# Optimization experiments

Measured on AMD Instinct MI355X. Metric: run time of the kernel, lower is better.

Reference implementation:

```python
import jax, jax.numpy as jnp
import numpy as np

ALPHA = 10.0   # args.alpha softmax sharpness
EPS = 1e-8     # torch CosineSimilarity eps


def setup_inputs() -> dict:
    key = jax.random.key(0)
    k0, k1, k2, k3 = jax.random.split(key, 4)
    B, S, F, D, C = 8, 1024, 32, 128, 16
    Hs = jax.random.normal(k0, (B, S, F, D), dtype=jnp.float32)
    Cj = jax.random.normal(k1, (C, D), dtype=jnp.float32)
    W = jax.random.normal(k2, (D, D), dtype=jnp.float32) * 0.05  # nn.Linear weight [out,in]
    b = jnp.zeros((D,), dtype=jnp.float32)
    importance = jax.random.uniform(k3, (B, S, F), dtype=jnp.float32)
    return {"Hs": Hs, "Cj": Cj, "W": W, "b": b, "importance": importance}


def reference(Hs, Cj, W, b, importance):
    # Hs: [B,S,F,D] features; Cj: [C,D] cluster centers; importance: [B,S,F]
    # Faithful to Model_DTSSOCC.assignment (importance is not None branch),
    # but avoids materializing the broadcasted [B,S,F,C,D] repeat tensors.
    Hn = Hs / jnp.maximum(jnp.linalg.norm(Hs, axis=-1, keepdims=True), EPS)
    Cn = Cj / jnp.maximum(jnp.linalg.norm(Cj, axis=-1, keepdims=True), EPS)
    cos = jnp.einsum('bsfd,cd->bsfc', Hn, Cn)            # cosine_sim4 over dim D
    logits = -ALPHA * 0.5 * (1.0 - cos)                  # -alpha * dists, [B,S,F,C]
    w3 = jax.nn.softmax(logits, axis=3)                  # softmax over centers
    w = jax.nn.softmax(logits, axis=2)                   # softmax over feas
    w3 = jnp.swapaxes(w3, 2, 3)                          # [B,S,C,F]
    w = jnp.swapaxes(w, 2, 3)                            # [B,S,C,F]
    F_tj = jax.nn.relu(jnp.einsum('bsfd,ed->bsfe', Hs, W) + b)  # relu(Linear(F_t))
    # importance update: bmm(w3, importance) then softmax over centers
    imp = jax.nn.softmax(jnp.einsum('bscf,bsf->bsc', w3, importance), axis=2)
    # weighted feature aggregation: bmm(w, F_tj) -> [B,S,C,D]
    f_t_new = jnp.einsum('bscf,bsfd->bscd', w, F_tj)
    return f_t_new, imp
```

## Files before the change

### kernel.cpp

```cpp
#include <hip/hip_runtime.h>
#include <hip/hip_bf16.h>
#include <math.h>

constexpr int Bn = 8, Sn = 1024, Fn = 32, Dn = 128, Cc = 16;
constexpr int NSITE = Bn * Sn;

#define EPSV 1e-8f

typedef __attribute__((ext_vector_type(8))) short bf16x8;
typedef __attribute__((ext_vector_type(4))) short bf16x4;
typedef __attribute__((ext_vector_type(4))) float f32x4;

__device__ inline short f2bf(float x) {
    __hip_bfloat16 h = __float2bfloat16(x);
    short s;
    __builtin_memcpy(&s, &h, sizeof(s));
    return s;
}

__device__ inline bf16x8 cvt8(f32x4 x0, f32x4 x1) {
    bf16x8 r;
    r[0] = f2bf(x0[0]); r[1] = f2bf(x0[1]); r[2] = f2bf(x0[2]); r[3] = f2bf(x0[3]);
    r[4] = f2bf(x1[0]); r[5] = f2bf(x1[1]); r[6] = f2bf(x1[2]); r[7] = f2bf(x1[3]);
    return r;
}

__global__ void prep_kernel(const float* __restrict__ Cj,
                            const float* __restrict__ W,
                            short* __restrict__ CnPack,
                            short* __restrict__ Wb) {
    const int tid = threadIdx.x;
    if (blockIdx.x < 64) {
        int t = blockIdx.x * 256 + tid;
        int n = t >> 7, k = t & 127;
        short v = f2bf(W[n * Dn + k]);
        int frag = (n >> 4) * 4 + (k >> 5);
        int lane = ((k >> 3) & 3) * 16 + (n & 15);
        Wb[(frag * 64 + lane) * 8 + (k & 7)] = v;
    } else {
        int c = blockIdx.x - 64;
        __shared__ float part[2];
        float v = 0.f, sq = 0.f;
        if (tid < 128) {
            v = Cj[c * Dn + tid];
            sq = v * v;
            #pragma unroll
            for (int off = 32; off > 0; off >>= 1) sq += __shfl_down(sq, off);
        }
        if (tid < 128 && (tid & 63) == 0) part[tid >> 6] = sq;
        __syncthreads();
        if (tid < 128) {
            float cn = v / fmaxf(sqrtf(part[0] + part[1]), EPSV);
            int kt = tid >> 5, ln = ((tid >> 3) & 3) * 16 + c, j = tid & 7;
            CnPack[(kt * 64 + ln) * 8 + j] = f2bf(cn);
        }
    }
}

__launch_bounds__(64, 4)
__global__ void site_kernel(const float* __restrict__ Hs,
                            const short* __restrict__ CnPack,
                            const short* __restrict__ Wb,
                            const float* __restrict__ bvec,
                            const float* __restrict__ imp_in,
                            float* __restrict__ f_out,
                            float* __restrict__ imp_out) {
    __shared__ __align__(16) short F_tjT[128][40];

    const int lane = threadIdx.x;
    const int c16  = lane & 15;
    const int g    = lane >> 4;
    const int site = blockIdx.x;

    const float* hsrc = Hs + (size_t)site * (Fn * Dn);
    const f32x4 zro = {0.f, 0.f, 0.f, 0.f};

    f32x4 x[16];
    #pragma unroll
    for (int kt = 0; kt < 4; ++kt) {
        const f32x4* p0 = (const f32x4*)(hsrc + c16 * Dn + kt * 32 + g * 8);
        const f32x4* p1 = (const f32x4*)(hsrc + (16 + c16) * Dn + kt * 32 + g * 8);
        x[4 * kt + 0] = p0[0];
        x[4 * kt + 1] = p0[1];
        x[4 * kt + 2] = p1[0];
        x[4 * kt + 3] = p1[1];
    }
    bf16x8 bcf[4];
    #pragma unroll
    for (int kt = 0; kt < 4; ++kt)
        bcf[kt] = *(const bf16x8*)&CnPack[(kt * 64 + lane) * 8];
    const float* impp = imp_in + (size_t)site * Fn;
    f32x4 impv0 = *(const f32x4*)(impp + 4 * g);
    f32x4 impv1 = *(const f32x4*)(impp + 16 + 4 * g);

    bf16x8 aF[2][4];
    #pragma unroll
    for (int kt = 0; kt < 4; ++kt) {
        aF[0][kt] = cvt8(x[4 * kt + 0], x[4 * kt + 1]);
        aF[1][kt] = cvt8(x[4 * kt + 2], x[4 * kt + 3]);
    }

    f32x4 gm0 = zro, gm1 = zro, cos0 = zro, cos1 = zro;
    #pragma unroll
    for (int kt = 0; kt < 4; ++kt) {
        gm0  = __builtin_amdgcn_mfma_f32_16x16x32_bf16(aF[0][kt], aF[0][kt], gm0, 0, 0, 0);
        gm1  = __builtin_amdgcn_mfma_f32_16x16x32_bf16(aF[1][kt], aF[1][kt], gm1, 0, 0, 0);
        cos0 = __builtin_amdgcn_mfma_f32_16x16x32_bf16(aF[0][kt], bcf[kt], cos0, 0, 0, 0);
        cos1 = __builtin_amdgcn_mfma_f32_16x16x32_bf16(aF[1][kt], bcf[kt], cos1, 0, 0, 0);
    }

    float s0[4], s1[4];
    #pragma unroll
    for (int r = 0; r < 4; ++r) {
        float q0 = __shfl(gm0[r], 20 * g + r);
        float q1 = __shfl(gm1[r], 20 * g + r);
        float i0 = 1.0f / fmaxf(sqrtf(q0), EPSV);
        float i1 = 1.0f / fmaxf(sqrtf(q1), EPSV);
        s0[r] = 5.0f * cos0[r] * i0;
        s1[r] = 5.0f * cos1[r] * i1;
    }

    bf16x8 wB;
    {
        float m = s0[0];
        #pragma unroll
        for (int r = 0; r < 4; ++r) { m = fmaxf(m, s0[r]); m = fmaxf(m, s1[r]); }
        m = fmaxf(m, __shfl_xor(m, 16));
        m = fmaxf(m, __shfl_xor(m, 32));
        float e0[4], e1[4], sum = 0.f;
        #pragma unroll
        for (int r = 0; r < 4; ++r) {
            e0[r] = __expf(s0[r] - m); e1[r] = __expf(s1[r] - m);
            sum += e0[r] + e1[r];
        }
        sum += __shfl_xor(sum, 16);
        sum += __shfl_xor(sum, 32);
        float inv = 1.0f / sum;
        #pragma unroll
        for (int r = 0; r < 4; ++r) { e0[r] *= inv; e1[r] *= inv; }
        const int srcA = c16 + 16 * ((2 * g) & 3);
        const int srcB = c16 + 16 * ((2 * g + 1) & 3);
        const bool hi = (g >= 2);
        #pragma unroll
        for (int r = 0; r < 4; ++r) {
            float a0 = __shfl(e0[r], srcA);
            float a1 = __shfl(e1[r], srcA);
            wB[r] = f2bf(hi ? a1 : a0);
            float b0 = __shfl(e0[r], srcB);
            float b1 = __shfl(e1[r], srcB);
            wB[4 + r] = f2bf(hi ? b1 : b0);
        }
    }

    {
        float t = 0.f;
        #pragma unroll
        for (int h = 0; h < 2; ++h) {
            #pragma unroll
            for (int r = 0; r < 4; ++r) {
                float sv = h ? s1[r] : s0[r];
                float m3 = sv;
                m3 = fmaxf(m3, __shfl_xor(m3, 1));
                m3 = fmaxf(m3, __shfl_xor(m3, 2));
                m3 = fmaxf(m3, __shfl_xor(m3, 4));
                m3 = fmaxf(m3, __shfl_xor(m3, 8));
                float e3 = __expf(sv - m3);
                float q3 = e3;
                q3 += __shfl_xor(q3, 1);
                q3 += __shfl_xor(q3, 2);
                q3 += __shfl_xor(q3, 4);
                q3 += __shfl_xor(q3, 8);
                t += (e3 / q3) * (h ? impv1[r] : impv0[r]);
            }
        }
        t += __shfl_xor(t, 16);
        t += __shfl_xor(t, 32);
        float mi = t;
        mi = fmaxf(mi, __shfl_xor(mi, 1));
        mi = fmaxf(mi, __shfl_xor(mi, 2));
        mi = fmaxf(mi, __shfl_xor(mi, 4));
        mi = fmaxf(mi, __shfl_xor(mi, 8));
        float ei = __expf(t - mi);
        float si = ei;
        si += __shfl_xor(si, 1);
        si += __shfl_xor(si, 2);
        si += __shfl_xor(si, 4);
        si += __shfl_xor(si, 8);
        if (g == 0) imp_out[(size_t)site * Cc + c16] = ei / si;
    }

    #pragma unroll
    for (int nt = 0; nt < 8; ++nt) {
        bf16x8 bw0 = *(const bf16x8*)&Wb[((nt * 4) + 0) * 512 + lane * 8];
        bf16x8 bw1 = *(const bf16x8*)&Wb[((nt * 4) + 1) * 512 + lane * 8];
        bf16x8 bw2 = *(const bf16x8*)&Wb[((nt * 4) + 2) * 512 + lane * 8];
        bf16x8 bw3 = *(const bf16x8*)&Wb[((nt * 4) + 3) * 512 + lane * 8];
        f32x4 acc0 = zro, acc1 = zro;
        acc0 = __builtin_amdgcn_mfma_f32_16x16x32_bf16(aF[0][0], bw0, acc0, 0, 0, 0);
        acc1 = __builtin_amdgcn_mfma_f32_16x16x32_bf16(aF[1][0], bw0, acc1, 0, 0, 0);
        acc0 = __builtin_amdgcn_mfma_f32_16x16x32_bf16(aF[0][1], bw1, acc0, 0, 0, 0);
        acc1 = __builtin_amdgcn_mfma_f32_16x16x32_bf16(aF[1][1], bw1, acc1, 0, 0, 0);
        acc0 = __builtin_amdgcn_mfma_f32_16x16x32_bf16(aF[0][2], bw2, acc0, 0, 0, 0);
        acc1 = __builtin_amdgcn_mfma_f32_16x16x32_bf16(aF[1][2], bw2, acc1, 0, 0, 0);
        acc0 = __builtin_amdgcn_mfma_f32_16x16x32_bf16(aF[0][3], bw3, acc0, 0, 0, 0);
        acc1 = __builtin_amdgcn_mfma_f32_16x16x32_bf16(aF[1][3], bw3, acc1, 0, 0, 0);
        float bb = bvec[nt * 16 + c16];
        bf16x4 p0, p1;
        #pragma unroll
        for (int r = 0; r < 4; ++r) {
            p0[r] = f2bf(fmaxf(acc0[r] + bb, 0.f));
            p1[r] = f2bf(fmaxf(acc1[r] + bb, 0.f));
        }
        *(bf16x4*)&F_tjT[nt * 16 + c16][4 * g]      = p0;
        *(bf16x4*)&F_tjT[nt * 16 + c16][16 + 4 * g] = p1;
    }

    {
        float* op = f_out + (size_t)site * (Cc * Dn);
        #pragma unroll
        for (int nt = 0; nt < 8; ++nt) {
            bf16x8 aFt = *(const bf16x8*)&F_tjT[nt * 16 + c16][8 * g];
            f32x4 o = __builtin_amdgcn_mfma_f32_16x16x32_bf16(aFt, wB, zro, 0, 0, 0);
            *(f32x4*)(op + c16 * Dn + nt * 16 + 4 * g) = o;
        }
    }
}

extern "C" void kernel_launch(void* const* d_in, const int* in_sizes, int n_in,
                              void* d_out, int out_size, void* d_ws, size_t ws_size,
                              hipStream_t stream) {
    const float* Hs  = (const float*)d_in[0];
    const float* Cj  = (const float*)d_in[1];
    const float* W   = (const float*)d_in[2];
    const float* b   = (const float*)d_in[3];
    const float* imp = (const float*)d_in[4];

    float* f_out   = (float*)d_out;
    float* imp_out = f_out + (size_t)NSITE * Cc * Dn;

    short* CnPack = (short*)d_ws;
    short* Wb     = CnPack + Cc * Dn;

    hipLaunchKernelGGL(prep_kernel, dim3(80), dim3(256), 0, stream, Cj, W, CnPack, Wb);
    hipLaunchKernelGGL(site_kernel, dim3(NSITE), dim3(64), 0, stream,
                       Hs, CnPack, Wb, b, imp, f_out, imp_out);
}
```

Measured before the change: 47.08 us.

## Process two sites per wavefront with prefetched loads for the second site

Each 64-thread block now handles two consecutive sites. It issues all Hs and importance loads for both sites up front, interleaved with the bf16 conversion, then runs the per-site compute twice. Bias values are hoisted into registers and reused across both sites. The aim is more memory-level parallelism and less per-block overhead. The cost is higher register pressure, so launch bounds drop to 3 waves per SIMD and the grid is halved.

```diff
diff --git a/kernel.cpp b/kernel.cpp
--- a/kernel.cpp
+++ b/kernel.cpp
@@ -57,7 +57,7 @@
     }
 }
 
-__launch_bounds__(64, 4)
+__launch_bounds__(64, 3)
 __global__ void site_kernel(const float* __restrict__ Hs,
                             const short* __restrict__ CnPack,
                             const short* __restrict__ Wb,
@@ -70,160 +70,198 @@
     const int lane = threadIdx.x;
     const int c16  = lane & 15;
     const int g    = lane >> 4;
-    const int site = blockIdx.x;
-
-    const float* hsrc = Hs + (size_t)site * (Fn * Dn);
+    const int siteA = blockIdx.x * 2;
+    const int siteB = siteA + 1;
+
     const f32x4 zro = {0.f, 0.f, 0.f, 0.f};
 
-    f32x4 x[16];
-    #pragma unroll
-    for (int kt = 0; kt < 4; ++kt) {
-        const f32x4* p0 = (const f32x4*)(hsrc + c16 * Dn + kt * 32 + g * 8);
-        const f32x4* p1 = (const f32x4*)(hsrc + (16 + c16) * Dn + kt * 32 + g * 8);
-        x[4 * kt + 0] = p0[0];
-        x[4 * kt + 1] = p0[1];
-        x[4 * kt + 2] = p1[0];
-        x[4 * kt + 3] = p1[1];
-    }
     bf16x8 bcf[4];
     #pragma unroll
     for (int kt = 0; kt < 4; ++kt)
         bcf[kt] = *(const bf16x8*)&CnPack[(kt * 64 + lane) * 8];
-    const float* impp = imp_in + (size_t)site * Fn;
-    f32x4 impv0 = *(const f32x4*)(impp + 4 * g);
-    f32x4 impv1 = *(const f32x4*)(impp + 16 + 4 * g);
-
-    bf16x8 aF[2][4];
+    float biasv[8];
+    #pragma unroll
+    for (int nt = 0; nt < 8; ++nt) biasv[nt] = bvec[nt * 16 + c16];
+
+    const float* impA = imp_in + (size_t)siteA * Fn;
+    const float* impB = imp_in + (size_t)siteB * Fn;
+    f32x4 impA0 = *(const f32x4*)(impA + 4 * g);
+    f32x4 impA1 = *(const f32x4*)(impA + 16 + 4 * g);
+    f32x4 impB0 = *(const f32x4*)(impB + 4 * g);
+    f32x4 impB1 = *(const f32x4*)(impB + 16 + 4 * g);
+
+    const float* hA = Hs + (size_t)siteA * (Fn * Dn);
+    const float* hB = Hs + (size_t)siteB * (Fn * Dn);
+    f32x4 xA[16], xB[16];
     #pragma unroll
     for (int kt = 0; kt < 4; ++kt) {
-        aF[0][kt] = cvt8(x[4 * kt + 0], x[4 * kt + 1]);
-        aF[1][kt] = cvt8(x[4 * kt + 2], x[4 * kt + 3]);
-    }
-
-    f32x4 gm0 = zro, gm1 = zro, cos0 = zro, cos1 = zro;
+        const f32x4* p0 = (const f32x4*)(hA + c16 * Dn + kt * 32 + g * 8);
+        const f32x4* p1 = (const f32x4*)(hA + (16 + c16) * Dn + kt * 32 + g * 8);
+        xA[4 * kt + 0] = p0[0];
+        xA[4 * kt + 1] = p0[1];
+        xA[4 * kt + 2] = p1[0];
+        xA[4 * kt + 3] = p1[1];
+    }
+    #pragma unroll
+    for (int kt = 0; kt < 2; ++kt) {
+        const f32x4* p0 = (const f32x4*)(hB + c16 * Dn + kt * 32 + g * 8);
+        const f32x4* p1 = (const f32x4*)(hB + (16 + c16) * Dn + kt * 32 + g * 8);
+        xB[4 * kt + 0] = p0[0];
+        xB[4 * kt + 1] = p0[1];
+        xB[4 * kt + 2] = p1[0];
+        xB[4 * kt + 3] = p1[1];
+    }
+    bf16x8 aFA[2][4], aFB[2][4];
     #pragma unroll
     for (int kt = 0; kt < 4; ++kt) {
-        gm0  = __builtin_amdgcn_mfma_f32_16x16x32_bf16(aF[0][kt], aF[0][kt], gm0, 0, 0, 0);
-        gm1  = __builtin_amdgcn_mfma_f32_16x16x32_bf16(aF[1][kt], aF[1][kt], gm1, 0, 0, 0);
-        cos0 = __builtin_amdgcn_mfma_f32_16x16x32_bf16(aF[0][kt], bcf[kt], cos0, 0, 0, 0);
-        cos1 = __builtin_amdgcn_mfma_f32_16x16x32_bf16(aF[1][kt], bcf[kt], cos1, 0, 0, 0);
-    }
-
-    float s0[4], s1[4];
-    #pragma unroll
-    for (int r = 0; r < 4; ++r) {
-        float q0 = __shfl(gm0[r], 20 * g + r);
-        float q1 = __shfl(gm1[r], 20 * g + r);
-        float i0 = 1.0f / fmaxf(sqrtf(q0), EPSV);
-        float i1 = 1.0f / fmaxf(sqrtf(q1), EPSV);
-        s0[r] = 5.0f * cos0[r] * i0;
-        s1[r] = 5.0f * cos1[r] * i1;
-    }
-
-    bf16x8 wB;
-    {
-        float m = s0[0];
+        aFA[0][kt] = cvt8(xA[4 * kt + 0], xA[4 * kt + 1]);
+        aFA[1][kt] = cvt8(xA[4 * kt + 2], xA[4 * kt + 3]);
+    }
+    #pragma unroll
+    for (int kt = 2; kt < 4; ++kt) {
+        const f32x4* p0 = (const f32x4*)(hB + c16 * Dn + kt * 32 + g * 8);
+        const f32x4* p1 = (const f32x4*)(hB + (16 + c16) * Dn + kt * 32 + g * 8);
+        xB[4 * kt + 0] = p0[0];
+        xB[4 * kt + 1] = p0[1];
+        xB[4 * kt + 2] = p1[0];
+        xB[4 * kt + 3] = p1[1];
+    }
+    #pragma unroll
+    for (int kt = 0; kt < 4; ++kt) {
+        aFB[0][kt] = cvt8(xB[4 * kt + 0], xB[4 * kt + 1]);
+        aFB[1][kt] = cvt8(xB[4 * kt + 2], xB[4 * kt + 3]);
+    }
+
+    auto do_site = [&](int site, const bf16x8 (&aF)[2][4],
+                       const f32x4& impv0, const f32x4& impv1) {
+        f32x4 gm0 = zro, gm1 = zro, cos0 = zro, cos1 = zro;
         #pragma unroll
-        for (int r = 0; r < 4; ++r) { m = fmaxf(m, s0[r]); m = fmaxf(m, s1[r]); }
-        m = fmaxf(m, __shfl_xor(m, 16));
-        m = fmaxf(m, __shfl_xor(m, 32));
-        float e0[4], e1[4], sum = 0.f;
+        for (int kt = 0; kt < 4; ++kt) {
+            gm0  = __builtin_amdgcn_mfma_f32_16x16x32_bf16(aF[0][kt], aF[0][kt], gm0, 0, 0, 0);
+            gm1  = __builtin_amdgcn_mfma_f32_16x16x32_bf16(aF[1][kt], aF[1][kt], gm1, 0, 0, 0);
+            cos0 = __builtin_amdgcn_mfma_f32_16x16x32_bf16(aF[0][kt], bcf[kt], cos0, 0, 0, 0);
+            cos1 = __builtin_amdgcn_mfma_f32_16x16x32_bf16(aF[1][kt], bcf[kt], cos1, 0, 0, 0);
+        }
+
+        float s0[4], s1[4];
         #pragma unroll
         for (int r = 0; r < 4; ++r) {
-            e0[r] = __expf(s0[r] - m); e1[r] = __expf(s1[r] - m);
-            sum += e0[r] + e1[r];
-        }
-        sum += __shfl_xor(sum, 16);
-        sum += __shfl_xor(sum, 32);
-        float inv = 1.0f / sum;
-        #pragma unroll
-        for (int r = 0; r < 4; ++r) { e0[r] *= inv; e1[r] *= inv; }
-        const int srcA = c16 + 16 * ((2 * g) & 3);
-        const int srcB = c16 + 16 * ((2 * g + 1) & 3);
-        const bool hi = (g >= 2);
-        #pragma unroll
-        for (int r = 0; r < 4; ++r) {
-            float a0 = __shfl(e0[r], srcA);
-            float a1 = __shfl(e1[r], srcA);
-            wB[r] = f2bf(hi ? a1 : a0);
-            float b0 = __shfl(e0[r], srcB);
-            float b1 = __shfl(e1[r], srcB);
-            wB[4 + r] = f2bf(hi ? b1 : b0);
-        }
-    }
-
-    {
-        float t = 0.f;
-        #pragma unroll
-        for (int h = 0; h < 2; ++h) {
+            float q0 = __shfl(gm0[r], 20 * g + r);
+            float q1 = __shfl(gm1[r], 20 * g + r);
+            float i0 = 1.0f / fmaxf(sqrtf(q0), EPSV);
+            float i1 = 1.0f / fmaxf(sqrtf(q1), EPSV);
+            s0[r] = 5.0f * cos0[r] * i0;
+            s1[r] = 5.0f * cos1[r] * i1;
+        }
+
+        bf16x8 wB;
+        {
+            float m = s0[0];
+            #pragma unroll
+            for (int r = 0; r < 4; ++r) { m = fmaxf(m, s0[r]); m = fmaxf(m, s1[r]); }
+            m = fmaxf(m, __shfl_xor(m, 16));
+            m = fmaxf(m, __shfl_xor(m, 32));
+            float e0[4], e1[4], sum = 0.f;
             #pragma unroll
             for (int r = 0; r < 4; ++r) {
-                float sv = h ? s1[r] : s0[r];
-                float m3 = sv;
-                m3 = fmaxf(m3, __shfl_xor(m3, 1));
-                m3 = fmaxf(m3, __shfl_xor(m3, 2));
-                m3 = fmaxf(m3, __shfl_xor(m3, 4));
-                m3 = fmaxf(m3, __shfl_xor(m3, 8));
-                float e3 = __expf(sv - m3);
-                float q3 = e3;
-                q3 += __shfl_xor(q3, 1);
-                q3 += __shfl_xor(q3, 2);
-                q3 += __shfl_xor(q3, 4);
-                q3 += __shfl_xor(q3, 8);
-                t += (e3 / q3) * (h ? impv1[r] : impv0[r]);
-            }
-        }
-        t += __shfl_xor(t, 16);
-        t += __shfl_xor(t, 32);
-        float mi = t;
-        mi = fmaxf(mi, __shfl_xor(mi, 1));
-        mi = fmaxf(mi, __shfl_xor(mi, 2));
-        mi = fmaxf(mi, __shfl_xor(mi, 4));
-        mi = fmaxf(mi, __shfl_xor(mi, 8));
-        float ei = __expf(t - mi);
-        float si = ei;
-        si += __shfl_xor(si, 1);
-        si += __shfl_xor(si, 2);
-        si += __shfl_xor(si, 4);
-        si += __shfl_xor(si, 8);
-        if (g == 0) imp_out[(size_t)site * Cc + c16] = ei / si;
-    }
-
-    #pragma unroll
-    for (int nt = 0; nt < 8; ++nt) {
-        bf16x8 bw0 = *(const bf16x8*)&Wb[((nt * 4) + 0) * 512 + lane * 8];
-        bf16x8 bw1 = *(const bf16x8*)&Wb[((nt * 4) + 1) * 512 + lane * 8];
-        bf16x8 bw2 = *(const bf16x8*)&Wb[((nt * 4) + 2) * 512 + lane * 8];
-        bf16x8 bw3 = *(const bf16x8*)&Wb[((nt * 4) + 3) * 512 + lane * 8];
-        f32x4 acc0 = zro, acc1 = zro;
-        acc0 = __builtin_amdgcn_mfma_f32_16x16x32_bf16(aF[0][0], bw0, acc0, 0, 0, 0);
-        acc1 = __builtin_amdgcn_mfma_f32_16x16x32_bf16(aF[1][0], bw0, acc1, 0, 0, 0);
-        acc0 = __builtin_amdgcn_mfma_f32_16x16x32_bf16(aF[0][1], bw1, acc0, 0, 0, 0);
-        acc1 = __builtin_amdgcn_mfma_f32_16x16x32_bf16(aF[1][1], bw1, acc1, 0, 0, 0);
-        acc0 = __builtin_amdgcn_mfma_f32_16x16x32_bf16(aF[0][2], bw2, acc0, 0, 0, 0);
-        acc1 = __builtin_amdgcn_mfma_f32_16x16x32_bf16(aF[1][2], bw2, acc1, 0, 0, 0);
-        acc0 = __builtin_amdgcn_mfma_f32_16x16x32_bf16(aF[0][3], bw3, acc0, 0, 0, 0);
-        acc1 = __builtin_amdgcn_mfma_f32_16x16x32_bf16(aF[1][3], bw3, acc1, 0, 0, 0);
-        float bb = bvec[nt * 16 + c16];
-        bf16x4 p0, p1;
-        #pragma unroll
-        for (int r = 0; r < 4; ++r) {
-            p0[r] = f2bf(fmaxf(acc0[r] + bb, 0.f));
-            p1[r] = f2bf(fmaxf(acc1[r] + bb, 0.f));
-        }
-        *(bf16x4*)&F_tjT[nt * 16 + c16][4 * g]      = p0;
-        *(bf16x4*)&F_tjT[nt * 16 + c16][16 + 4 * g] = p1;
-    }
-
-    {
-        float* op = f_out + (size_t)site * (Cc * Dn);
+                e0[r] = __expf(s0[r] - m); e1[r] = __expf(s1[r] - m);
+                sum += e0[r] + e1[r];
+            }
+            sum += __shfl_xor(sum, 16);
+            sum += __shfl_xor(sum, 32);
+            float inv = 1.0f / sum;
+            #pragma unroll
+            for (int r = 0; r < 4; ++r) { e0[r] *= inv; e1[r] *= inv; }
+            const int srcA = c16 + 16 * ((2 * g) & 3);
+            const int srcB = c16 + 16 * ((2 * g + 1) & 3);
+            const bool hi = (g >= 2);
+            #pragma unroll
+            for (int r = 0; r < 4; ++r) {
+                float a0 = __shfl(e0[r], srcA);
+                float a1 = __shfl(e1[r], srcA);
+                wB[r] = f2bf(hi ? a1 : a0);
+                float b0 = __shfl(e0[r], srcB);
+                float b1 = __shfl(e1[r], srcB);
+                wB[4 + r] = f2bf(hi ? b1 : b0);
+            }
+        }
+
+        {
+            float t = 0.f;
+            #pragma unroll
+            for (int h = 0; h < 2; ++h) {
+                #pragma unroll
+                for (int r = 0; r < 4; ++r) {
+                    float sv = h ? s1[r] : s0[r];
+                    float m3 = sv;
+                    m3 = fmaxf(m3, __shfl_xor(m3, 1));
+                    m3 = fmaxf(m3, __shfl_xor(m3, 2));
+                    m3 = fmaxf(m3, __shfl_xor(m3, 4));
+                    m3 = fmaxf(m3, __shfl_xor(m3, 8));
+                    float e3 = __expf(sv - m3);
+                    float q3 = e3;
+                    q3 += __shfl_xor(q3, 1);
+                    q3 += __shfl_xor(q3, 2);
+                    q3 += __shfl_xor(q3, 4);
+                    q3 += __shfl_xor(q3, 8);
+                    t += (e3 / q3) * (h ? impv1[r] : impv0[r]);
+                }
+            }
+            t += __shfl_xor(t, 16);
+            t += __shfl_xor(t, 32);
+            float mi = t;
+            mi = fmaxf(mi, __shfl_xor(mi, 1));
+            mi = fmaxf(mi, __shfl_xor(mi, 2));
+            mi = fmaxf(mi, __shfl_xor(mi, 4));
+            mi = fmaxf(mi, __shfl_xor(mi, 8));
+            float ei = __expf(t - mi);
+            float si = ei;
+            si += __shfl_xor(si, 1);
+            si += __shfl_xor(si, 2);
+            si += __shfl_xor(si, 4);
+            si += __shfl_xor(si, 8);
+            if (g == 0) imp_out[(size_t)site * Cc + c16] = ei / si;
+        }
+
         #pragma unroll
         for (int nt = 0; nt < 8; ++nt) {
-            bf16x8 aFt = *(const bf16x8*)&F_tjT[nt * 16 + c16][8 * g];
-            f32x4 o = __builtin_amdgcn_mfma_f32_16x16x32_bf16(aFt, wB, zro, 0, 0, 0);
-            *(f32x4*)(op + c16 * Dn + nt * 16 + 4 * g) = o;
-        }
-    }
+            bf16x8 bw0 = *(const bf16x8*)&Wb[((nt * 4) + 0) * 512 + lane * 8];
+            bf16x8 bw1 = *(const bf16x8*)&Wb[((nt * 4) + 1) * 512 + lane * 8];
+            bf16x8 bw2 = *(const bf16x8*)&Wb[((nt * 4) + 2) * 512 + lane * 8];
+            bf16x8 bw3 = *(const bf16x8*)&Wb[((nt * 4) + 3) * 512 + lane * 8];
+            f32x4 acc0 = zro, acc1 = zro;
+            acc0 = __builtin_amdgcn_mfma_f32_16x16x32_bf16(aF[0][0], bw0, acc0, 0, 0, 0);
+            acc1 = __builtin_amdgcn_mfma_f32_16x16x32_bf16(aF[1][0], bw0, acc1, 0, 0, 0);
+            acc0 = __builtin_amdgcn_mfma_f32_16x16x32_bf16(aF[0][1], bw1, acc0, 0, 0, 0);
+            acc1 = __builtin_amdgcn_mfma_f32_16x16x32_bf16(aF[1][1], bw1, acc1, 0, 0, 0);
+            acc0 = __builtin_amdgcn_mfma_f32_16x16x32_bf16(aF[0][2], bw2, acc0, 0, 0, 0);
+            acc1 = __builtin_amdgcn_mfma_f32_16x16x32_bf16(aF[1][2], bw2, acc1, 0, 0, 0);
+            acc0 = __builtin_amdgcn_mfma_f32_16x16x32_bf16(aF[0][3], bw3, acc0, 0, 0, 0);
+            acc1 = __builtin_amdgcn_mfma_f32_16x16x32_bf16(aF[1][3], bw3, acc1, 0, 0, 0);
+            float bb = biasv[nt];
+            bf16x4 p0, p1;
+            #pragma unroll
+            for (int r = 0; r < 4; ++r) {
+                p0[r] = f2bf(fmaxf(acc0[r] + bb, 0.f));
+                p1[r] = f2bf(fmaxf(acc1[r] + bb, 0.f));
+            }
+            *(bf16x4*)&F_tjT[nt * 16 + c16][4 * g]      = p0;
+            *(bf16x4*)&F_tjT[nt * 16 + c16][16 + 4 * g] = p1;
+        }
+
+        {
+            float* op = f_out + (size_t)site * (Cc * Dn);
+            #pragma unroll
+            for (int nt = 0; nt < 8; ++nt) {
+                bf16x8 aFt = *(const bf16x8*)&F_tjT[nt * 16 + c16][8 * g];
+                f32x4 o = __builtin_amdgcn_mfma_f32_16x16x32_bf16(aFt, wB, zro, 0, 0, 0);
+                *(f32x4*)(op + c16 * Dn + nt * 16 + 4 * g) = o;
+            }
+        }
+    };
+
+    do_site(siteA, aFA, impA0, impA1);
+    do_site(siteB, aFB, impB0, impB1);
 }
 
 extern "C" void kernel_launch(void* const* d_in, const int* in_sizes, int n_in,
@@ -242,6 +280,6 @@
     short* Wb     = CnPack + Cc * Dn;
 
     hipLaunchKernelGGL(prep_kernel, dim3(80), dim3(256), 0, stream, Cj, W, CnPack, Wb);
-    hipLaunchKernelGGL(site_kernel, dim3(NSITE), dim3(64), 0, stream,
+    hipLaunchKernelGGL(site_kernel, dim3(NSITE / 2), dim3(64), 0, stream,
                        Hs, CnPack, Wb, b, imp, f_out, imp_out);
 }
```

Result: slower. 62.91 us (+33.6%).

## Pack four sites per block and replace LDS transpose with lane shuffles

Applied to the files above, without the earlier changes.

Launches 256-thread blocks handling four sites (one per wave) instead of one 64-thread block per site, with launch bounds raised for higher occupancy. The shared-memory transpose of the relu(linear) output is replaced by packed bf16 pairs exchanged via cross-lane shuffles before the aggregation MFMA. Hs loads are split into two halves and the other operand loads moved nearer their use to lower register pressure. This trades LDS traffic and barrier-free per-site blocks for extra shuffles and possibly less memory-level parallelism per wave.

```diff
diff --git a/kernel.cpp b/kernel.cpp
--- a/kernel.cpp
+++ b/kernel.cpp
@@ -8,7 +8,6 @@
 #define EPSV 1e-8f
 
 typedef __attribute__((ext_vector_type(8))) short bf16x8;
-typedef __attribute__((ext_vector_type(4))) short bf16x4;
 typedef __attribute__((ext_vector_type(4))) float f32x4;
 
 __device__ inline short f2bf(float x) {
@@ -16,6 +15,11 @@
     short s;
     __builtin_memcpy(&s, &h, sizeof(s));
     return s;
+}
+
+__device__ inline unsigned pk2(float lo, float hi) {
+    return (unsigned)(unsigned short)f2bf(lo) |
+           ((unsigned)(unsigned short)f2bf(hi) << 16);
 }
 
 __device__ inline bf16x8 cvt8(f32x4 x0, f32x4 x1) {
@@ -57,7 +61,7 @@
     }
 }
 
-__launch_bounds__(64, 4)
+__launch_bounds__(256, 8)
 __global__ void site_kernel(const float* __restrict__ Hs,
                             const short* __restrict__ CnPack,
                             const short* __restrict__ Wb,
@@ -65,48 +69,49 @@
                             const float* __restrict__ imp_in,
                             float* __restrict__ f_out,
                             float* __restrict__ imp_out) {
-    __shared__ __align__(16) short F_tjT[128][40];
-
-    const int lane = threadIdx.x;
+    const int lane = threadIdx.x & 63;
+    const int wv   = threadIdx.x >> 6;
     const int c16  = lane & 15;
     const int g    = lane >> 4;
-    const int site = blockIdx.x;
+    const int site = blockIdx.x * 4 + wv;
 
     const float* hsrc = Hs + (size_t)site * (Fn * Dn);
     const f32x4 zro = {0.f, 0.f, 0.f, 0.f};
 
-    f32x4 x[16];
+    const int srcA = c16 + 16 * ((2 * g) & 3);
+    const int srcB = c16 + 16 * ((2 * g + 1) & 3);
+    const bool hi  = (g >= 2);
+
+    bf16x8 aF0[4], aF1[4];
+    #pragma unroll
+    for (int kp = 0; kp < 2; ++kp) {
+        f32x4 x[8];
+        #pragma unroll
+        for (int k2 = 0; k2 < 2; ++k2) {
+            int kt = 2 * kp + k2;
+            const f32x4* p0 = (const f32x4*)(hsrc + c16 * Dn + kt * 32 + g * 8);
+            const f32x4* p1 = (const f32x4*)(hsrc + (16 + c16) * Dn + kt * 32 + g * 8);
+            x[4 * k2 + 0] = p0[0];
+            x[4 * k2 + 1] = p0[1];
+            x[4 * k2 + 2] = p1[0];
+            x[4 * k2 + 3] = p1[1];
+        }
+        #pragma unroll
+        for (int k2 = 0; k2 < 2; ++k2) {
+            int kt = 2 * kp + k2;
+            aF0[kt] = cvt8(x[4 * k2 + 0], x[4 * k2 + 1]);
+            aF1[kt] = cvt8(x[4 * k2 + 2], x[4 * k2 + 3]);
+        }
+    }
+
+    f32x4 gm0 = zro, gm1 = zro, cos0 = zro, cos1 = zro;
     #pragma unroll
     for (int kt = 0; kt < 4; ++kt) {
-        const f32x4* p0 = (const f32x4*)(hsrc + c16 * Dn + kt * 32 + g * 8);
-        const f32x4* p1 = (const f32x4*)(hsrc + (16 + c16) * Dn + kt * 32 + g * 8);
-        x[4 * kt + 0] = p0[0];
-        x[4 * kt + 1] = p0[1];
-        x[4 * kt + 2] = p1[0];
-        x[4 * kt + 3] = p1[1];
-    }
-    bf16x8 bcf[4];
-    #pragma unroll
-    for (int kt = 0; kt < 4; ++kt)
-        bcf[kt] = *(const bf16x8*)&CnPack[(kt * 64 + lane) * 8];
-    const float* impp = imp_in + (size_t)site * Fn;
-    f32x4 impv0 = *(const f32x4*)(impp + 4 * g);
-    f32x4 impv1 = *(const f32x4*)(impp + 16 + 4 * g);
-
-    bf16x8 aF[2][4];
-    #pragma unroll
-    for (int kt = 0; kt < 4; ++kt) {
-        aF[0][kt] = cvt8(x[4 * kt + 0], x[4 * kt + 1]);
-        aF[1][kt] = cvt8(x[4 * kt + 2], x[4 * kt + 3]);
-    }
-
-    f32x4 gm0 = zro, gm1 = zro, cos0 = zro, cos1 = zro;
-    #pragma unroll
-    for (int kt = 0; kt < 4; ++kt) {
-        gm0  = __builtin_amdgcn_mfma_f32_16x16x32_bf16(aF[0][kt], aF[0][kt], gm0, 0, 0, 0);
-        gm1  = __builtin_amdgcn_mfma_f32_16x16x32_bf16(aF[1][kt], aF[1][kt], gm1, 0, 0, 0);
-        cos0 = __builtin_amdgcn_mfma_f32_16x16x32_bf16(aF[0][kt], bcf[kt], cos0, 0, 0, 0);
-        cos1 = __builtin_amdgcn_mfma_f32_16x16x32_bf16(aF[1][kt], bcf[kt], cos1, 0, 0, 0);
+        bf16x8 bc = *(const bf16x8*)&CnPack[(kt * 64 + lane) * 8];
+        gm0  = __builtin_amdgcn_mfma_f32_16x16x32_bf16(aF0[kt], aF0[kt], gm0, 0, 0, 0);
+        gm1  = __builtin_amdgcn_mfma_f32_16x16x32_bf16(aF1[kt], aF1[kt], gm1, 0, 0, 0);
+        cos0 = __builtin_amdgcn_mfma_f32_16x16x32_bf16(aF0[kt], bc, cos0, 0, 0, 0);
+        cos1 = __builtin_amdgcn_mfma_f32_16x16x32_bf16(aF1[kt], bc, cos1, 0, 0, 0);
     }
 
     float s0[4], s1[4];
@@ -138,9 +143,6 @@
         float inv = 1.0f / sum;
         #pragma unroll
         for (int r = 0; r < 4; ++r) { e0[r] *= inv; e1[r] *= inv; }
-        const int srcA = c16 + 16 * ((2 * g) & 3);
-        const int srcB = c16 + 16 * ((2 * g + 1) & 3);
-        const bool hi = (g >= 2);
         #pragma unroll
         for (int r = 0; r < 4; ++r) {
             float a0 = __shfl(e0[r], srcA);
@@ -153,6 +155,9 @@
     }
 
     {
+        const float* impp = imp_in + (size_t)site * Fn;
+        f32x4 impv0 = *(const f32x4*)(impp + 4 * g);
+        f32x4 impv1 = *(const f32x4*)(impp + 16 + 4 * g);
         float t = 0.f;
         #pragma unroll
         for (int h = 0; h < 2; ++h) {
@@ -189,40 +194,36 @@
         if (g == 0) imp_out[(size_t)site * Cc + c16] = ei / si;
     }
 
+    float* op = f_out + (size_t)site * (Cc * Dn) + c16 * Dn;
     #pragma unroll
     for (int nt = 0; nt < 8; ++nt) {
-        bf16x8 bw0 = *(const bf16x8*)&Wb[((nt * 4) + 0) * 512 + lane * 8];
-        bf16x8 bw1 = *(const bf16x8*)&Wb[((nt * 4) + 1) * 512 + lane * 8];
-        bf16x8 bw2 = *(const bf16x8*)&Wb[((nt * 4) + 2) * 512 + lane * 8];
-        bf16x8 bw3 = *(const bf16x8*)&Wb[((nt * 4) + 3) * 512 + lane * 8];
         f32x4 acc0 = zro, acc1 = zro;
-        acc0 = __builtin_amdgcn_mfma_f32_16x16x32_bf16(aF[0][0], bw0, acc0, 0, 0, 0);
-        acc1 = __builtin_amdgcn_mfma_f32_16x16x32_bf16(aF[1][0], bw0, acc1, 0, 0, 0);
-        acc0 = __builtin_amdgcn_mfma_f32_16x16x32_bf16(aF[0][1], bw1, acc0, 0, 0, 0);
-        acc1 = __builtin_amdgcn_mfma_f32_16x16x32_bf16(aF[1][1], bw1, acc1, 0, 0, 0);
-        acc0 = __builtin_amdgcn_mfma_f32_16x16x32_bf16(aF[0][2], bw2, acc0, 0, 0, 0);
-        acc1 = __builtin_amdgcn_mfma_f32_16x16x32_bf16(aF[1][2], bw2, acc1, 0, 0, 0);
-        acc0 = __builtin_amdgcn_mfma_f32_16x16x32_bf16(aF[0][3], bw3, acc0, 0, 0, 0);
-        acc1 = __builtin_amdgcn_mfma_f32_16x16x32_bf16(aF[1][3], bw3, acc1, 0, 0, 0);
+        #pragma unroll
+        for (int kp = 0; kp < 2; ++kp) {
+            bf16x8 bwA = *(const bf16x8*)&Wb[((nt * 4) + 2 * kp + 0) * 512 + lane * 8];
+            bf16x8 bwB = *(const bf16x8*)&Wb[((nt * 4) + 2 * kp + 1) * 512 + lane * 8];
+            acc0 = __builtin_amdgcn_mfma_f32_16x16x32_bf16(aF0[2 * kp + 0], bwA, acc0, 0, 0, 0);
+            acc1 = __builtin_amdgcn_mfma_f32_16x16x32_bf16(aF1[2 * kp + 0], bwA, acc1, 0, 0, 0);
+            acc0 = __builtin_amdgcn_mfma_f32_16x16x32_bf16(aF0[2 * kp + 1], bwB, acc0, 0, 0, 0);
+            acc1 = __builtin_amdgcn_mfma_f32_16x16x32_bf16(aF1[2 * kp + 1], bwB, acc1, 0, 0, 0);
+        }
         float bb = bvec[nt * 16 + c16];
-        bf16x4 p0, p1;
-        #pragma unroll
-        for (int r = 0; r < 4; ++r) {
-            p0[r] = f2bf(fmaxf(acc0[r] + bb, 0.f));
-            p1[r] = f2bf(fmaxf(acc1[r] + bb, 0.f));
-        }
-        *(bf16x4*)&F_tjT[nt * 16 + c16][4 * g]      = p0;
-        *(bf16x4*)&F_tjT[nt * 16 + c16][16 + 4 * g] = p1;
-    }
-
-    {
-        float* op = f_out + (size_t)site * (Cc * Dn);
-        #pragma unroll
-        for (int nt = 0; nt < 8; ++nt) {
-            bf16x8 aFt = *(const bf16x8*)&F_tjT[nt * 16 + c16][8 * g];
-            f32x4 o = __builtin_amdgcn_mfma_f32_16x16x32_bf16(aFt, wB, zro, 0, 0, 0);
-            *(f32x4*)(op + c16 * Dn + nt * 16 + 4 * g) = o;
-        }
+        unsigned q0a = pk2(fmaxf(acc0[0] + bb, 0.f), fmaxf(acc0[1] + bb, 0.f));
+        unsigned q0b = pk2(fmaxf(acc0[2] + bb, 0.f), fmaxf(acc0[3] + bb, 0.f));
+        unsigned q1a = pk2(fmaxf(acc1[0] + bb, 0.f), fmaxf(acc1[1] + bb, 0.f));
+        unsigned q1b = pk2(fmaxf(acc1[2] + bb, 0.f), fmaxf(acc1[3] + bb, 0.f));
+        int t0, t1;
+        union { bf16x8 v; int u[4]; } fr;
+        t0 = __shfl((int)q0a, srcA); t1 = __shfl((int)q1a, srcA);
+        fr.u[0] = hi ? t1 : t0;
+        t0 = __shfl((int)q0b, srcA); t1 = __shfl((int)q1b, srcA);
+        fr.u[1] = hi ? t1 : t0;
+        t0 = __shfl((int)q0a, srcB); t1 = __shfl((int)q1a, srcB);
+        fr.u[2] = hi ? t1 : t0;
+        t0 = __shfl((int)q0b, srcB); t1 = __shfl((int)q1b, srcB);
+        fr.u[3] = hi ? t1 : t0;
+        f32x4 o = __builtin_amdgcn_mfma_f32_16x16x32_bf16(fr.v, wB, zro, 0, 0, 0);
+        *(f32x4*)(op + nt * 16 + 4 * g) = o;
     }
 }
 
@@ -242,6 +243,6 @@
     short* Wb     = CnPack + Cc * Dn;
 
     hipLaunchKernelGGL(prep_kernel, dim3(80), dim3(256), 0, stream, Cj, W, CnPack, Wb);
-    hipLaunchKernelGGL(site_kernel, dim3(NSITE), dim3(64), 0, stream,
+    hipLaunchKernelGGL(site_kernel, dim3(NSITE / 4), dim3(256), 0, stream,
                        Hs, CnPack, Wb, b, imp, f_out, imp_out);
 }
```

Result: slower. 89.04 us (+89.1%).
